# Performance work log

Measured on AMD Instinct MI355X. Metric: run time of the kernel, lower is better.

The kernel has to match this reference:

```python
import jax, jax.numpy as jnp
import numpy as np

K = 8  # kernel_size
COUT = 512


def setup_inputs() -> dict:
    key = jax.random.key(0)
    k1, k2, k3 = jax.random.split(key, 3)
    B, CIN, L = 8, 512, 2048
    x = jax.random.normal(k1, (B, CIN, L), dtype=jnp.float32)
    # nn.Linear(CIN, COUT*K) weight, scaled like kaiming-uniform-ish init
    W = jax.random.normal(k2, (COUT * K, CIN), dtype=jnp.float32) * (1.0 / np.sqrt(CIN))
    b = jax.random.normal(k3, (COUT,), dtype=jnp.float32)
    return {"x": x, "W": W, "b": b}


def reference(x, W, b):
    # x: (B, Cin, L); W: (Cout*K, Cin) with row layout j = k*Cout + co; b: (Cout,)
    B, Cin, L = x.shape
    # pointwise linear expand: (B, Cout*K, L)
    z = jnp.einsum('bcl,oc->bol', x, W)
    z = z.reshape(B, K, COUT, L)  # k-major channel layout
    # causal overlap-add fold: y[b,co,t] = sum_k z[b,k,co,t-k]
    y = z[:, 0]
    for k in range(1, K):  # small fixed kernel-size loop
        y = y.at[:, :, k:].add(z[:, k, :, : L - k])
    return y + b[None, :, None]
```

## Files before the change

kernel.cpp:

```cpp
#include <hip/hip_runtime.h>
#include <hip/hip_bf16.h>
#include <cstdint>
#include <cstddef>

#define CIN   512
#define COUT  512
#define LLEN  2048
#define BATCH 8
#define KTAP  8
#define LPAD  (LLEN + 8)

typedef __bf16 bf16x8_t __attribute__((ext_vector_type(8)));
typedef float  f32x4_t  __attribute__((ext_vector_type(4)));
typedef unsigned short u16x8_t __attribute__((ext_vector_type(8)));

__device__ __forceinline__ unsigned short f2bf(float f) {
  __bf16 h = (__bf16)f;
  return __builtin_bit_cast(unsigned short, h);
}

__device__ __forceinline__ void gl2lds16(unsigned short* lds, const unsigned short* g) {
  __builtin_amdgcn_global_load_lds(
      (const __attribute__((address_space(1))) unsigned int*)g,
      (__attribute__((address_space(3))) unsigned int*)lds,
      16, 0, 0);
}

__global__ __launch_bounds__(256) void prepass_kernel(
    const float* __restrict__ x, unsigned short* __restrict__ xtp,
    const float4* __restrict__ W, u16x8_t* __restrict__ Wf) {
  const int bid = blockIdx.x;
  const int t   = threadIdx.x;

  if (bid >= 2048) {
    int idx = (bid - 2048) * 256 + t;
    float4 a = W[idx * 2], b = W[idx * 2 + 1];
    u16x8_t o;
    o[0] = f2bf(a.x); o[1] = f2bf(a.y); o[2] = f2bf(a.z); o[3] = f2bf(a.w);
    o[4] = f2bf(b.x); o[5] = f2bf(b.y); o[6] = f2bf(b.z); o[7] = f2bf(b.w);
    const int row  = idx >> 6;
    const int cch  = idx & 63;
    const int k    = row >> 9, oo = row & 511;
    const int o128 = oo >> 7, wm = (oo >> 6) & 1, fi = (oo >> 4) & 3, lrow = oo & 15;
    const int ct   = cch >> 3, chin = cch & 7, hg = chin >> 2, quad = chin & 3;
    const int lane = quad * 16 + lrow;
    const int off  = k * 32768 + o128 * 8192 + wm * 4096 + hg * 2048 +
                     ct * 256 + fi * 64 + lane;
    Wf[off] = o;
    return;
  }

  __shared__ float tile[64][65];
  const int b  = bid >> 8;
  const int c0 = ((bid >> 5) & 7) * 64;
  const int l0 = (bid & 31) * 64;

  if ((bid & 31) == 0 && t < 64) {
    unsigned short* hp = xtp + ((size_t)b * LPAD + (t >> 3)) * CIN + c0 + (t & 7) * 8;
    *(u16x8_t*)hp = (u16x8_t){0, 0, 0, 0, 0, 0, 0, 0};
  }

  {
    const int cr = t >> 2;
    const int lv = (t & 3) * 16;
    const float* src = x + ((size_t)b * CIN + c0 + cr) * LLEN + l0 + lv;
#pragma unroll
    for (int i = 0; i < 4; ++i) {
      float4 v = *(const float4*)(src + 4 * i);
      tile[cr][lv + 4 * i + 0] = v.x;
      tile[cr][lv + 4 * i + 1] = v.y;
      tile[cr][lv + 4 * i + 2] = v.z;
      tile[cr][lv + 4 * i + 3] = v.w;
    }
  }
  __syncthreads();
  {
    const int l    = t >> 2;
    const int cseg = (t & 3) * 16;
    unsigned short ov[16];
#pragma unroll
    for (int u = 0; u < 16; ++u) ov[u] = f2bf(tile[cseg + u][l]);
    unsigned short* dst = xtp + ((size_t)b * LPAD + 8 + l0 + l) * CIN + c0 + cseg;
    *(u16x8_t*)dst       = *(const u16x8_t*)&ov[0];
    *(u16x8_t*)(dst + 8) = *(const u16x8_t*)&ov[8];
  }
}


__global__ __launch_bounds__(512, 4) void conv_gemm_kernel(
    const unsigned short* __restrict__ Wf,
    const unsigned short* __restrict__ xtp,
    const float* __restrict__ bias,
    float* __restrict__ y)
{
  __shared__ __align__(16) unsigned char smem[65536];

  const int t    = threadIdx.x;
  const int lane = t & 63;
  const int wid  = t >> 6;
  const int wm   = wid & 1;
  const int wn   = (wid >> 1) & 1;
  const int hg   = wid >> 2;
  const int l0   = blockIdx.x * 128;
  const int o0   = blockIdx.y * 128;
  const int b    = blockIdx.z;

  const int quad = lane >> 4;
  const int lrow = lane & 15;

  unsigned short* BsBuf = (unsigned short*)smem;

  f32x4_t acc[4][4];
#pragma unroll
  for (int i = 0; i < 4; ++i)
#pragma unroll
    for (int j = 0; j < 4; ++j)
      acc[i][j] = (f32x4_t){0.f, 0.f, 0.f, 0.f};

  const int srow    = t >> 3;
  const int schunk  = (t & 7) ^ (srow & 7);
  const int lds_off = t * 8;

  const unsigned short* xb = xtp + (size_t)b * LPAD * CIN;

  auto stage_B = [&](int ct, int buf) {
    const int c0 = ct * 64;
    const unsigned short* src = xb + (size_t)(l0 + srow) * CIN + c0 + schunk * 8;
#pragma unroll
    for (int rd = 0; rd < 2; ++rd)
      gl2lds16(BsBuf + buf * 8704 + lds_off + rd * 4096, src + (size_t)rd * 64 * CIN);
    if (t < 64) {
      const int r2  = 128 + (t >> 3);
      const int ch2 = (t & 7) ^ (r2 & 7);
      gl2lds16(BsBuf + buf * 8704 + 128 * 64 + t * 8,
               xb + (size_t)(l0 + r2) * CIN + c0 + ch2 * 8);
    }
  };

  const u16x8_t* Wfp = (const u16x8_t*)Wf;
  const int woff = blockIdx.y * 8192 + wm * 4096 + hg * 2048 + lane;

  stage_B(0, 0);
  __syncthreads();

#pragma unroll 1
  for (int ct = 0; ct < 8; ++ct) {
    if (ct + 1 < 8) stage_B(ct + 1, (ct + 1) & 1);
    const unsigned short* Bc = BsBuf + (ct & 1) * 8704;
    const u16x8_t* wp = Wfp + woff + ct * 256;
#pragma unroll
    for (int k = 0; k < 8; ++k) {
      bf16x8_t af[4], bfr[4];
#pragma unroll
      for (int i = 0; i < 4; ++i)
        af[i] = __builtin_bit_cast(bf16x8_t, wp[k * 32768 + i * 64]);
#pragma unroll
      for (int j = 0; j < 4; ++j) {
        int row  = (8 - k) + wn * 64 + j * 16 + lrow;
        int slot = (hg * 4 + quad) ^ (row & 7);
        bfr[j] = *(const bf16x8_t*)(Bc + row * 64 + slot * 8);
      }
      __builtin_amdgcn_s_setprio(1);
#pragma unroll
      for (int i = 0; i < 4; ++i)
#pragma unroll
        for (int j = 0; j < 4; ++j)
          acc[i][j] = __builtin_amdgcn_mfma_f32_16x16x32_bf16(af[i], bfr[j], acc[i][j], 0, 0, 0);
      __builtin_amdgcn_s_setprio(0);
    }
    __syncthreads();
  }

  float* red = (float*)smem + (size_t)(wn * 2 + wm) * 4096;
  if (hg == 1) {
#pragma unroll
    for (int i = 0; i < 4; ++i)
#pragma unroll
      for (int j = 0; j < 4; ++j)
#pragma unroll
        for (int r = 0; r < 4; ++r)
          red[((i * 4 + j) * 4 + r) * 64 + lane] = acc[i][j][r];
  }
  __syncthreads();
  if (hg == 0) {
#pragma unroll
    for (int i = 0; i < 4; ++i) {
      const int o_base = o0 + wm * 64 + i * 16 + quad * 4;
      const float4 bv = *(const float4*)(bias + o_base);
      const float bvr[4] = {bv.x, bv.y, bv.z, bv.w};
#pragma unroll
      for (int j = 0; j < 4; ++j) {
        const int l = l0 + wn * 64 + j * 16 + lrow;
#pragma unroll
        for (int r = 0; r < 4; ++r) {
          float v = acc[i][j][r] + red[((i * 4 + j) * 4 + r) * 64 + lane];
          y[((size_t)b * COUT + o_base + r) * LLEN + l] = v + bvr[r];
        }
      }
    }
  }
}


extern "C" void kernel_launch(void* const* d_in, const int* in_sizes, int n_in,
                              void* d_out, int out_size, void* d_ws, size_t ws_size,
                              hipStream_t stream) {
  const float* x    = (const float*)d_in[0];
  const float* W    = (const float*)d_in[1];
  const float* bias = (const float*)d_in[2];
  float* y          = (float*)d_out;

  unsigned short* xtp = (unsigned short*)d_ws;
  unsigned short* Wf  = (unsigned short*)((char*)d_ws +
                        (size_t)BATCH * LPAD * CIN * sizeof(unsigned short));

  prepass_kernel<<<2048 + 1024, 256, 0, stream>>>(
      x, xtp, (const float4*)W, (u16x8_t*)Wf);
  conv_gemm_kernel<<<dim3(LLEN / 128, COUT / 128, BATCH), 512, 0, stream>>>(
      Wf, xtp, bias, y);
}
```

Before: 144.8 us.

## Enlarge prepass transpose tiles and swizzle GEMM block order across XCDs

Result: slower. 148.0 us (+2.2%).

```diff
diff --git a/kernel.cpp b/kernel.cpp
--- a/kernel.cpp
+++ b/kernel.cpp
@@ -32,8 +32,8 @@
   const int bid = blockIdx.x;
   const int t   = threadIdx.x;
 
-  if (bid >= 2048) {
-    int idx = (bid - 2048) * 256 + t;
+  if (bid >= 512) {
+    int idx = (bid - 512) * 256 + t;
     float4 a = W[idx * 2], b = W[idx * 2 + 1];
     u16x8_t o;
     o[0] = f2bf(a.x); o[1] = f2bf(a.y); o[2] = f2bf(a.z); o[3] = f2bf(a.w);
@@ -50,39 +50,43 @@
     return;
   }
 
-  __shared__ float tile[64][65];
-  const int b  = bid >> 8;
-  const int c0 = ((bid >> 5) & 7) * 64;
-  const int l0 = (bid & 31) * 64;
-
-  if ((bid & 31) == 0 && t < 64) {
+  __shared__ float tile[64][140];
+  const int b     = bid >> 6;
+  const int rem   = bid & 63;
+  const int c0    = (rem >> 3) * 64;
+  const int lbase = (rem & 7) * 256;
+
+  if ((rem & 7) == 0 && t < 64) {
     unsigned short* hp = xtp + ((size_t)b * LPAD + (t >> 3)) * CIN + c0 + (t & 7) * 8;
     *(u16x8_t*)hp = (u16x8_t){0, 0, 0, 0, 0, 0, 0, 0};
   }
 
-  {
-    const int cr = t >> 2;
-    const int lv = (t & 3) * 16;
-    const float* src = x + ((size_t)b * CIN + c0 + cr) * LLEN + l0 + lv;
-#pragma unroll
-    for (int i = 0; i < 4; ++i) {
-      float4 v = *(const float4*)(src + 4 * i);
-      tile[cr][lv + 4 * i + 0] = v.x;
-      tile[cr][lv + 4 * i + 1] = v.y;
-      tile[cr][lv + 4 * i + 2] = v.z;
-      tile[cr][lv + 4 * i + 3] = v.w;
-    }
-  }
-  __syncthreads();
-  {
-    const int l    = t >> 2;
-    const int cseg = (t & 3) * 16;
-    unsigned short ov[16];
-#pragma unroll
-    for (int u = 0; u < 16; ++u) ov[u] = f2bf(tile[cseg + u][l]);
-    unsigned short* dst = xtp + ((size_t)b * LPAD + 8 + l0 + l) * CIN + c0 + cseg;
-    *(u16x8_t*)dst       = *(const u16x8_t*)&ov[0];
-    *(u16x8_t*)(dst + 8) = *(const u16x8_t*)&ov[8];
+#pragma unroll 1
+  for (int p = 0; p < 2; ++p) {
+    const int l0 = lbase + p * 128;
+    {
+      const int cr = t >> 2;
+      const float* srcp = x + ((size_t)b * CIN + c0 + cr) * LLEN + l0;
+#pragma unroll
+      for (int i = 0; i < 8; ++i) {
+        float4 v = *(const float4*)(srcp + ((t & 3) + 4 * i) * 4);
+        *(float4*)&tile[cr][((t & 3) + 4 * i) * 4] = v;
+      }
+    }
+    __syncthreads();
+    {
+      const int l    = t >> 1;
+      const int cseg = (t & 1) * 32;
+      unsigned short ov[32];
+#pragma unroll
+      for (int u = 0; u < 32; ++u) ov[u] = f2bf(tile[cseg + u][l]);
+      unsigned short* dst = xtp + ((size_t)b * LPAD + 8 + l0 + l) * CIN + c0 + cseg;
+      *(u16x8_t*)(dst)      = *(const u16x8_t*)&ov[0];
+      *(u16x8_t*)(dst + 8)  = *(const u16x8_t*)&ov[8];
+      *(u16x8_t*)(dst + 16) = *(const u16x8_t*)&ov[16];
+      *(u16x8_t*)(dst + 24) = *(const u16x8_t*)&ov[24];
+    }
+    __syncthreads();
   }
 }
 
@@ -95,15 +99,20 @@
 {
   __shared__ __align__(16) unsigned char smem[65536];
 
+  const int bid = blockIdx.x;
+  const int swz = (bid & 7) * 64 + (bid >> 3);
+  const int oy  = swz >> 7;
+  const int rzx = swz & 127;
+  const int b   = rzx >> 4;
+  const int l0  = (rzx & 15) * 128;
+  const int o0  = oy * 128;
+
   const int t    = threadIdx.x;
   const int lane = t & 63;
   const int wid  = t >> 6;
   const int wm   = wid & 1;
   const int wn   = (wid >> 1) & 1;
   const int hg   = wid >> 2;
-  const int l0   = blockIdx.x * 128;
-  const int o0   = blockIdx.y * 128;
-  const int b    = blockIdx.z;
 
   const int quad = lane >> 4;
   const int lrow = lane & 15;
@@ -138,7 +147,7 @@
   };
 
   const u16x8_t* Wfp = (const u16x8_t*)Wf;
-  const int woff = blockIdx.y * 8192 + wm * 4096 + hg * 2048 + lane;
+  const int woff = oy * 8192 + wm * 4096 + hg * 2048 + lane;
 
   stage_B(0, 0);
   __syncthreads();
@@ -165,7 +174,8 @@
       for (int i = 0; i < 4; ++i)
 #pragma unroll
         for (int j = 0; j < 4; ++j)
-          acc[i][j] = __builtin_amdgcn_mfma_f32_16x16x32_bf16(af[i], bfr[j], acc[i][j], 0, 0, 0);
+          acc[i][j] = __builtin_amdgcn_mfma_f32_16x16x32_bf16(
+              af[i], bfr[j], acc[i][j], 0, 0, 0);
       __builtin_amdgcn_s_setprio(0);
     }
     __syncthreads();
@@ -214,8 +224,8 @@
   unsigned short* Wf  = (unsigned short*)((char*)d_ws +
                         (size_t)BATCH * LPAD * CIN * sizeof(unsigned short));
 
-  prepass_kernel<<<2048 + 1024, 256, 0, stream>>>(
+  prepass_kernel<<<512 + 1024, 256, 0, stream>>>(
       x, xtp, (const float4*)W, (u16x8_t*)Wf);
-  conv_gemm_kernel<<<dim3(LLEN / 128, COUT / 128, BATCH), 512, 0, stream>>>(
+  conv_gemm_kernel<<<512, 512, 0, stream>>>(
       Wf, xtp, bias, y);
 }
```
